# Optimization experiments

Hardware: AMD Instinct MI355X
Metric: run time of the kernel (lower is better)

The kernel has to match this reference:

```python
import jax, jax.numpy as jnp
import numpy as np

DIM = 768
NUM_HEADS = 12
HEAD_DIM = DIM // NUM_HEADS
SCALE = HEAD_DIM ** -0.5


def setup_inputs() -> dict:
    key = jax.random.key(0)
    k1, k2, k3, k4, k5 = jax.random.split(key, 5)
    B, N = 2, 2048
    x = jax.random.normal(k1, (B, N, DIM), dtype=jnp.float32)
    # nn.Linear weights stored as [out, in]; we keep them as [in, out] for jnp use.
    Wq = jax.random.normal(k2, (DIM, DIM), dtype=jnp.float32) * (DIM ** -0.5)
    Wkv = jax.random.normal(k3, (DIM, 2 * HEAD_DIM), dtype=jnp.float32) * (DIM ** -0.5)
    Wproj = jax.random.normal(k4, (DIM, DIM), dtype=jnp.float32) * (DIM ** -0.5)
    bproj = jax.random.normal(k5, (DIM,), dtype=jnp.float32) * 0.01
    return {"x": x, "Wq": Wq, "Wkv": Wkv, "Wproj": Wproj, "bproj": bproj, "num_layer": 0}


def reference(x, Wq, Wkv, Wproj, bproj, num_layer):
    B, N, C = x.shape
    H, D = NUM_HEADS, HEAD_DIM
    q = (x @ Wq).reshape(B, N, H, D).transpose(0, 2, 1, 3)        # [B,H,N,D]
    kv = (x @ Wkv).reshape(B, N, 2, D)
    k, v = kv[:, :, 0, :], kv[:, :, 1, :]                          # [B,N,D] shared across heads (MQA)
    attn = jnp.einsum('bhid,bjd->bhij', q, k) * SCALE              # [B,H,N,N]
    attn = jax.nn.softmax(attn, axis=-1)
    out = jnp.einsum('bhij,bjd->bhid', attn, v)                    # [B,H,N,D]
    out = out.transpose(0, 2, 1, 3).reshape(B, N, C)
    return out @ Wproj + bproj
```

## Files before the change

kernel.cpp:

```cpp
#include <hip/hip_runtime.h>

#define BATCH 2
#define SEQ   2048
#define DIMC  768
#define HEADS 12
#define HD    64
#define QSCALE 0.1803368801111204f

typedef short bf16x8 __attribute__((ext_vector_type(8)));
typedef float f32x4  __attribute__((ext_vector_type(4)));
typedef float f32x16 __attribute__((ext_vector_type(16)));

__device__ __forceinline__ unsigned short f2bf(float f) {
    union { float f; unsigned int u; } a; a.f = f;
    unsigned int r = a.u + 0x7fffu + ((a.u >> 16) & 1u);
    return (unsigned short)(r >> 16);
}
__device__ __forceinline__ unsigned int pack2bf(float lo, float hi) {
    union { float f; unsigned int u; } a, b; a.f = lo; b.f = hi;
    return __builtin_amdgcn_perm(b.u + 0x8000u, a.u + 0x8000u, 0x07060302);
}
__device__ __forceinline__ unsigned int cvtpk_bf16(float lo, float hi) {
    unsigned int r;
    asm("v_cvt_pk_bf16_f32 %0, %1, %2" : "=v"(r) : "v"(lo), "v"(hi));
    return r;
}
__device__ __forceinline__ float exp2f_fast(float x) { return __builtin_amdgcn_exp2f(x); }

__device__ __forceinline__ void gload16(const unsigned short* g, unsigned short* l) {
    __builtin_amdgcn_global_load_lds(
        (const __attribute__((address_space(1))) unsigned int*)g,
        (__attribute__((address_space(3))) unsigned int*)l, 16, 0, 0);
}

__global__ void prep(const float* __restrict__ Wq, const float* __restrict__ Wkv,
                     const float* __restrict__ Wproj, const float* __restrict__ x,
                     unsigned short* __restrict__ WqT, unsigned short* __restrict__ WkvT,
                     unsigned short* __restrict__ WprT, unsigned short* __restrict__ xb)
{
    const int bid = blockIdx.x, t = threadIdx.x;
    if (bid >= 1248) {
        const size_t base = (size_t)(bid - 1248) * 2048 + (size_t)t * 8;
        float4 v0 = *(const float4*)&x[base];
        float4 v1 = *(const float4*)&x[base + 4];
        uint4 o = { pack2bf(v0.x, v0.y), pack2bf(v0.z, v0.w),
                    pack2bf(v1.x, v1.y), pack2bf(v1.z, v1.w) };
        *(uint4*)&xb[base] = o;
        return;
    }
    __shared__ float sT[32][33];
    const float* W; unsigned short* WT; int N, tb;
    if (bid < 576)      { W = Wq;    WT = WqT;  N = DIMC;   tb = bid; }
    else if (bid < 672) { W = Wkv;   WT = WkvT; N = 2 * HD; tb = bid - 576; }
    else                { W = Wproj; WT = WprT; N = DIMC;   tb = bid - 672; }
    const int tilesN = N / 32;
    const int k0 = (tb / tilesN) * 32, n0 = (tb - (tb / tilesN) * tilesN) * 32;
    const int r = t >> 3, c4 = (t & 7) * 4;
    float4 v = *(const float4*)&W[(size_t)(k0 + r) * N + n0 + c4];
    sT[c4 + 0][r] = v.x; sT[c4 + 1][r] = v.y; sT[c4 + 2][r] = v.z; sT[c4 + 3][r] = v.w;
    __syncthreads();
    ushort4 o = { f2bf(sT[r][c4]), f2bf(sT[r][c4 + 1]), f2bf(sT[r][c4 + 2]), f2bf(sT[r][c4 + 3]) };
    *(ushort4*)&WT[(size_t)(n0 + r) * 768 + k0 + c4] = o;
}

template <int MODE>
__global__ __launch_bounds__(256)
void gemm128(const unsigned short* __restrict__ A, const unsigned short* __restrict__ BT,
             const float* __restrict__ bias, void* __restrict__ C0,
             unsigned short* __restrict__ Kout, unsigned short* __restrict__ VTout)
{
    __shared__ __align__(16) unsigned short sA[2][128 * 128];
    __shared__ __align__(16) unsigned short sB[2][128 * 128];
    const int t = threadIdx.x, lane = t & 63, w = t >> 6;
    const int bm = blockIdx.y * 128, bn = blockIdx.x * 128;
    const int wm = (w >> 1) * 64, wn = (w & 1) * 64;

    const unsigned short* Apt = &A [(size_t)(bm + (lane >> 2)) * DIMC + (lane & 3) * 8];
    const unsigned short* Bpt = &BT[(size_t)(bn + (lane >> 2)) * DIMC + (lane & 3) * 8];

    auto stage = [&](int kt, int bf) {
        const int off = kt * 128;
        #pragma unroll
        for (int kc = 0; kc < 4; ++kc) {
            #pragma unroll
            for (int g = 0; g < 2; ++g) {
                const int rg = 2 * w + g;
                const size_t goff = (size_t)rg * 16 * DIMC + off + kc * 32;
                gload16(Apt + goff, &sA[bf][kc * 4096 + rg * 512]);
                gload16(Bpt + goff, &sB[bf][kc * 4096 + rg * 512]);
            }
        }
    };

    const int fr = lane & 15, fk = (lane >> 4) * 8;

    f32x4 acc[4][4] = {};

    stage(0, 0);
    __syncthreads();
    for (int kt = 0; kt < DIMC / 128; ++kt) {
        const int buf = kt & 1;
        if (kt + 1 < DIMC / 128) stage(kt + 1, buf ^ 1);
        #pragma unroll
        for (int kc = 0; kc < 4; ++kc) {
            bf16x8 af[4], bq[4];
            #pragma unroll
            for (int i = 0; i < 4; ++i)
                af[i] = *(const bf16x8*)&sA[buf][kc * 4096 + (wm + i * 16 + fr) * 32 + fk];
            #pragma unroll
            for (int j = 0; j < 4; ++j)
                bq[j] = *(const bf16x8*)&sB[buf][kc * 4096 + (wn + j * 16 + fr) * 32 + fk];
            #pragma unroll
            for (int i = 0; i < 4; ++i)
                #pragma unroll
                for (int j = 0; j < 4; ++j)
                    acc[i][j] = __builtin_amdgcn_mfma_f32_16x16x32_bf16(af[i], bq[j], acc[i][j], 0, 0, 0);
        }
        __syncthreads();
    }

    const int cn = lane & 15, cm = (lane >> 4) * 4;
    #pragma unroll
    for (int j = 0; j < 4; ++j) {
        const int n = bn + wn + j * 16 + cn;
        #pragma unroll
        for (int i = 0; i < 4; ++i) {
            #pragma unroll
            for (int r = 0; r < 4; ++r) {
                const int m = bm + wm + i * 16 + cm + r;
                float val = acc[i][j][r];
                if (MODE == 0) {
                    if (n < DIMC) {
                        ((unsigned short*)C0)[(size_t)m * DIMC + n] = f2bf(val * QSCALE);
                    } else {
                        const int c2 = n - DIMC;
                        if (c2 < HD) Kout[(size_t)m * HD + c2] = f2bf(val);
                        else {
                            const int bbk = m >> 11, tok = m & (SEQ - 1);
                            VTout[(size_t)bbk * HD * SEQ + (size_t)(c2 - HD) * SEQ + tok] = f2bf(val);
                        }
                    }
                } else {
                    ((float*)C0)[(size_t)m * DIMC + n] = val + bias[n];
                }
            }
        }
    }
}

__global__ __launch_bounds__(256)
void flash_kernel(const unsigned short* __restrict__ Qw, const unsigned short* __restrict__ Kw,
                  const unsigned short* __restrict__ VTw, unsigned short* __restrict__ Ob)
{
    const int qblk = blockIdx.x, h = blockIdx.y, b = blockIdx.z;
    const int tid = threadIdx.x, w = tid >> 6, lane = tid & 63;
    const int l31 = lane & 31, hi = lane >> 5;
    const int kr = w >> 1, qc = w & 1;

    __shared__ __align__(16) unsigned short sK [2][64][72];
    __shared__ __align__(16) unsigned short sVT[2][64][72];
    __shared__ float sL[4][32];
    __shared__ float sLi[2][32];

    const size_t qrow = (size_t)(b * SEQ + qblk * 64 + qc * 32 + l31);
    bf16x8 qf[4];
    #pragma unroll
    for (int s = 0; s < 4; ++s)
        qf[s] = *(const bf16x8*)&Qw[qrow * DIMC + h * HD + s * 16 + hi * 8];

    f32x16 oacc0 = {}, oacc1 = {};
    float lsum = 0.0f;

    const int r_st = tid >> 2, c_st = (tid & 3) * 16;
    const unsigned short* Kp  = &Kw[(size_t)(b * SEQ + r_st) * HD + c_st];
    const unsigned short* VTp = &VTw[(size_t)b * HD * SEQ + (size_t)r_st * SEQ + c_st];

    bf16x8 kg0, kg1, vg0, vg1;
    auto loadKV = [&](int ti) {
        const unsigned short* ks = Kp + (size_t)ti * 64 * HD;
        const unsigned short* vs = VTp + ti * 64;
        kg0 = *(const bf16x8*)&ks[0]; kg1 = *(const bf16x8*)&ks[8];
        vg0 = *(const bf16x8*)&vs[0]; vg1 = *(const bf16x8*)&vs[8];
    };
    auto writeKV = [&](int bf) {
        *(bf16x8*)&sK[bf][r_st][c_st]      = kg0;
        *(bf16x8*)&sK[bf][r_st][c_st + 8]  = kg1;
        *(bf16x8*)&sVT[bf][r_st][c_st]     = vg0;
        *(bf16x8*)&sVT[bf][r_st][c_st + 8] = vg1;
    };

    loadKV(0); writeKV(0); loadKV(1);
    __syncthreads();

    for (int kt = 0; kt < SEQ / 64; ++kt) {
        const int buf = kt & 1;
        if (kt + 1 < SEQ / 64) {
            writeKV(buf ^ 1);
            loadKV(kt + 2 < SEQ / 64 ? kt + 2 : SEQ / 64 - 1);
        }

        f32x16 st = {};
        __builtin_amdgcn_s_setprio(1);
        #pragma unroll
        for (int s = 0; s < 4; ++s) {
            bf16x8 ka = *(const bf16x8*)&sK[buf][kr * 32 + l31][s * 16 + hi * 8];
            st = __builtin_amdgcn_mfma_f32_32x32x16_bf16(ka, qf[s], st, 0, 0, 0);
        }
        __builtin_amdgcn_s_setprio(0);

        uint2 pg[4];
        #pragma unroll
        for (int g = 0; g < 4; ++g) {
            float p0 = exp2f_fast(st[g * 4 + 0]);
            float p1 = exp2f_fast(st[g * 4 + 1]);
            float p2 = exp2f_fast(st[g * 4 + 2]);
            float p3 = exp2f_fast(st[g * 4 + 3]);
            lsum += (p0 + p1) + (p2 + p3);
            pg[g].x = cvtpk_bf16(p0, p1);
            pg[g].y = cvtpk_bf16(p2, p3);
        }

        #pragma unroll
        for (int s = 0; s < 2; ++s) {
            unsigned int ax = pg[2 * s].x, bx = pg[2 * s + 1].x;
            unsigned int ay = pg[2 * s].y, by = pg[2 * s + 1].y;
            asm("v_permlane32_swap_b32 %0, %1" : "+v"(ax), "+v"(bx));
            asm("v_permlane32_swap_b32 %0, %1" : "+v"(ay), "+v"(by));
            union { uint4 u4; bf16x8 v; } pa;
            pa.u4.x = ax;
            pa.u4.y = ay;
            pa.u4.z = bx;
            pa.u4.w = by;
            bf16x8 vb0 = *(const bf16x8*)&sVT[buf][l31][kr * 32 + s * 16 + hi * 8];
            bf16x8 vb1 = *(const bf16x8*)&sVT[buf][32 + l31][kr * 32 + s * 16 + hi * 8];
            __builtin_amdgcn_s_setprio(1);
            oacc0 = __builtin_amdgcn_mfma_f32_32x32x16_bf16(pa.v, vb0, oacc0, 0, 0, 0);
            oacc1 = __builtin_amdgcn_mfma_f32_32x32x16_bf16(pa.v, vb1, oacc1, 0, 0, 0);
            __builtin_amdgcn_s_setprio(0);
        }
        __syncthreads();
    }

    lsum += __shfl_xor(lsum, 32);
    if (lane < 32) sL[w][l31] = lsum;

    float* scratch = (float*)&sK[0][0][0];
    {
        int rid = qc * 2 + (1 - kr);
        float* rg = scratch + rid * 1024;
        f32x16 give = kr ? oacc0 : oacc1;
        #pragma unroll
        for (int r = 0; r < 16; ++r) rg[r * 64 + lane] = give[r];
    }
    __syncthreads();

    f32x16 own = kr ? oacc1 : oacc0;
    {
        const float* rg = scratch + (qc * 2 + kr) * 1024;
        #pragma unroll
        for (int r = 0; r < 16; ++r) own[r] += rg[r * 64 + lane];
    }
    if (kr == 0 && lane < 32)
        sLi[qc][l31] = 1.0f / (sL[qc][l31] + sL[qc + 2][l31]);
    __syncthreads();

    #pragma unroll
    for (int r = 0; r < 16; ++r) {
        int rq = (r & 3) + 8 * (r >> 2) + 4 * hi;
        float iv = sLi[qc][rq];
        size_t row = (size_t)(b * SEQ + qblk * 64 + qc * 32 + rq);
        Ob[row * DIMC + h * HD + kr * 32 + l31] = f2bf(own[r] * iv);
    }
}

extern "C" void kernel_launch(void* const* d_in, const int* in_sizes, int n_in,
                              void* d_out, int out_size, void* d_ws, size_t ws_size,
                              hipStream_t stream)
{
    const float* x     = (const float*)d_in[0];
    const float* Wq    = (const float*)d_in[1];
    const float* Wkv   = (const float*)d_in[2];
    const float* Wproj = (const float*)d_in[3];
    const float* bproj = (const float*)d_in[4];

    const int M = BATCH * SEQ;
    unsigned short* WqT  = (unsigned short*)d_ws;
    unsigned short* WkvT = WqT  + DIMC * DIMC;
    unsigned short* WprT = WkvT + 2 * HD * DIMC;
    unsigned short* Qw   = WprT + DIMC * DIMC;
    unsigned short* Kw   = Qw   + (size_t)M * DIMC;
    unsigned short* VTw  = Kw   + (size_t)M * HD;
    unsigned short* Ob   = VTw  + (size_t)BATCH * HD * SEQ;
    unsigned short* xb   = Ob;

    prep<<<1248 + 1536, 256, 0, stream>>>(Wq, Wkv, Wproj, x, WqT, WkvT, WprT, xb);
    gemm128<0><<<dim3(7, M / 128), 256, 0, stream>>>(xb, WqT, nullptr, Qw, Kw, VTw);
    flash_kernel<<<dim3(SEQ / 64, HEADS, BATCH), 256, 0, stream>>>(Qw, Kw, VTw, Ob);
    gemm128<1><<<dim3(6, M / 128), 256, 0, stream>>>(Ob, WprT, bproj, d_out, nullptr, nullptr);
}
```

Before: 151.5 us.

## Load K/V tiles directly into registers, dropping shared-memory staging and barriers

The flash attention kernel no longer stages K and V^T tiles through double-buffered shared memory. Each wave loads its own MFMA operand fragments straight from global memory into registers, ping-ponging between two register sets, which removes the per-tile __syncthreads. Launch bounds now request three blocks per CU. The cost is redundant global loads, since K/V fragments are no longer shared across the waves that need them, plus higher register pressure from the two prefetch sets.

```diff
diff --git a/kernel.cpp b/kernel.cpp
--- a/kernel.cpp
+++ b/kernel.cpp
@@ -148,7 +148,7 @@
     }
 }
 
-__global__ __launch_bounds__(256)
+__global__ __launch_bounds__(256, 3)
 void flash_kernel(const unsigned short* __restrict__ Qw, const unsigned short* __restrict__ Kw,
                   const unsigned short* __restrict__ VTw, unsigned short* __restrict__ Ob)
 {
@@ -157,8 +157,7 @@
     const int l31 = lane & 31, hi = lane >> 5;
     const int kr = w >> 1, qc = w & 1;
 
-    __shared__ __align__(16) unsigned short sK [2][64][72];
-    __shared__ __align__(16) unsigned short sVT[2][64][72];
+    __shared__ float scratch[4][1024];
     __shared__ float sL[4][32];
     __shared__ float sLi[2][32];
 
@@ -171,41 +170,29 @@
     f32x16 oacc0 = {}, oacc1 = {};
     float lsum = 0.0f;
 
-    const int r_st = tid >> 2, c_st = (tid & 3) * 16;
-    const unsigned short* Kp  = &Kw[(size_t)(b * SEQ + r_st) * HD + c_st];
-    const unsigned short* VTp = &VTw[(size_t)b * HD * SEQ + (size_t)r_st * SEQ + c_st];
-
-    bf16x8 kg0, kg1, vg0, vg1;
-    auto loadKV = [&](int ti) {
-        const unsigned short* ks = Kp + (size_t)ti * 64 * HD;
-        const unsigned short* vs = VTp + ti * 64;
-        kg0 = *(const bf16x8*)&ks[0]; kg1 = *(const bf16x8*)&ks[8];
-        vg0 = *(const bf16x8*)&vs[0]; vg1 = *(const bf16x8*)&vs[8];
+    const unsigned short* Kbase = &Kw[((size_t)b * SEQ + kr * 32 + l31) * HD + hi * 8];
+    const unsigned short* V0b = &VTw[(size_t)b * HD * SEQ + (size_t)l31 * SEQ + kr * 32 + hi * 8];
+    const unsigned short* V1b = V0b + (size_t)32 * SEQ;
+
+    bf16x8 kA[4], kB[4], v0A[2], v1A[2], v0B[2], v1B[2];
+    auto loadT = [&](int kt, bf16x8* kf, bf16x8* v0, bf16x8* v1) {
+        const unsigned short* kp = Kbase + (size_t)kt * 64 * HD;
+        kf[0] = *(const bf16x8*)&kp[0];
+        kf[1] = *(const bf16x8*)&kp[16];
+        kf[2] = *(const bf16x8*)&kp[32];
+        kf[3] = *(const bf16x8*)&kp[48];
+        const unsigned short* vp0 = V0b + kt * 64;
+        const unsigned short* vp1 = V1b + kt * 64;
+        v0[0] = *(const bf16x8*)&vp0[0];  v0[1] = *(const bf16x8*)&vp0[16];
+        v1[0] = *(const bf16x8*)&vp1[0];  v1[1] = *(const bf16x8*)&vp1[16];
     };
-    auto writeKV = [&](int bf) {
-        *(bf16x8*)&sK[bf][r_st][c_st]      = kg0;
-        *(bf16x8*)&sK[bf][r_st][c_st + 8]  = kg1;
-        *(bf16x8*)&sVT[bf][r_st][c_st]     = vg0;
-        *(bf16x8*)&sVT[bf][r_st][c_st + 8] = vg1;
-    };
-
-    loadKV(0); writeKV(0); loadKV(1);
-    __syncthreads();
-
-    for (int kt = 0; kt < SEQ / 64; ++kt) {
-        const int buf = kt & 1;
-        if (kt + 1 < SEQ / 64) {
-            writeKV(buf ^ 1);
-            loadKV(kt + 2 < SEQ / 64 ? kt + 2 : SEQ / 64 - 1);
-        }
-
+
+    auto step = [&](const bf16x8* kf, const bf16x8* v0s, const bf16x8* v1s) {
         f32x16 st = {};
         __builtin_amdgcn_s_setprio(1);
         #pragma unroll
-        for (int s = 0; s < 4; ++s) {
-            bf16x8 ka = *(const bf16x8*)&sK[buf][kr * 32 + l31][s * 16 + hi * 8];
-            st = __builtin_amdgcn_mfma_f32_32x32x16_bf16(ka, qf[s], st, 0, 0, 0);
-        }
+        for (int s = 0; s < 4; ++s)
+            st = __builtin_amdgcn_mfma_f32_32x32x16_bf16(kf[s], qf[s], st, 0, 0, 0);
         __builtin_amdgcn_s_setprio(0);
 
         uint2 pg[4];
@@ -231,23 +218,27 @@
             pa.u4.y = ay;
             pa.u4.z = bx;
             pa.u4.w = by;
-            bf16x8 vb0 = *(const bf16x8*)&sVT[buf][l31][kr * 32 + s * 16 + hi * 8];
-            bf16x8 vb1 = *(const bf16x8*)&sVT[buf][32 + l31][kr * 32 + s * 16 + hi * 8];
             __builtin_amdgcn_s_setprio(1);
-            oacc0 = __builtin_amdgcn_mfma_f32_32x32x16_bf16(pa.v, vb0, oacc0, 0, 0, 0);
-            oacc1 = __builtin_amdgcn_mfma_f32_32x32x16_bf16(pa.v, vb1, oacc1, 0, 0, 0);
+            oacc0 = __builtin_amdgcn_mfma_f32_32x32x16_bf16(pa.v, v0s[s], oacc0, 0, 0, 0);
+            oacc1 = __builtin_amdgcn_mfma_f32_32x32x16_bf16(pa.v, v1s[s], oacc1, 0, 0, 0);
             __builtin_amdgcn_s_setprio(0);
         }
-        __syncthreads();
+    };
+
+    loadT(0, kA, v0A, v1A);
+    for (int kt = 0; kt < SEQ / 64; kt += 2) {
+        loadT(kt + 1, kB, v0B, v1B);
+        step(kA, v0A, v1A);
+        if (kt + 2 < SEQ / 64) loadT(kt + 2, kA, v0A, v1A);
+        step(kB, v0B, v1B);
     }
 
     lsum += __shfl_xor(lsum, 32);
     if (lane < 32) sL[w][l31] = lsum;
 
-    float* scratch = (float*)&sK[0][0][0];
     {
         int rid = qc * 2 + (1 - kr);
-        float* rg = scratch + rid * 1024;
+        float* rg = &scratch[rid][0];
         f32x16 give = kr ? oacc0 : oacc1;
         #pragma unroll
         for (int r = 0; r < 16; ++r) rg[r * 64 + lane] = give[r];
@@ -256,7 +247,7 @@
 
     f32x16 own = kr ? oacc1 : oacc0;
     {
-        const float* rg = scratch + (qc * 2 + kr) * 1024;
+        const float* rg = &scratch[qc * 2 + kr][0];
         #pragma unroll
         for (int r = 0; r < 16; ++r) own[r] += rg[r * 64 + lane];
     }
```

Result: slower. 202.9 us (+33.9%).
